# Optimization experiments

Measured on AMD Instinct MI355X. Metric: run time of the kernel, lower is better.

The kernel has to match this reference:

```python
import jax, jax.numpy as jnp
import numpy as np

H, W = 1024, 2048
K_CENTERS = 32          # fixed-size stand-in for torch.nonzero(center_heatmap > 0)
ROAD_ID = 0             # cityscapes trainId for 'road'
THING_START = 11        # cityscapes thing classes are trainIds >= 11
LABEL_DIVISOR = 1000
FILTER_IDS = (10, 19)   # 'sky', 'ego vehicle' depth filter classes
EPS = 1e-8


def _group_instances(heat, off, sem):
    # heat: (H,W) f32, off: (2,H,W) f32 [dy,dx], sem: (1,H,W) int
    vals, idx = jax.lax.top_k(heat.reshape(-1), K_CENTERS)
    cy = (idx // W).astype(jnp.float32)
    cx = (idx % W).astype(jnp.float32)
    valid = vals > 0.0
    ys = jnp.arange(H, dtype=jnp.float32)[:, None] + off[0]   # (H,W)
    xs = jnp.arange(W, dtype=jnp.float32)[None, :] + off[1]   # (H,W)
    d2 = (ys[None] - cy[:, None, None]) ** 2 + (xs[None] - cx[:, None, None]) ** 2  # (K,H,W)
    d2 = jnp.where(valid[:, None, None], d2, jnp.inf)
    inst = (jnp.argmin(d2, axis=0) + 1).astype(sem.dtype)     # (H,W), 1-based instance ids
    thing = sem >= THING_START
    any_valid = jnp.any(valid)
    return jnp.where(thing & any_valid, sem * LABEL_DIVISOR + inst[None], sem)


def _surface_normal(p):
    # p: (1,3,H,W) camera-space points; central-difference cross-product stencil
    px = jnp.pad(p, ((0, 0), (0, 0), (0, 0), (1, 1)), mode='edge')
    py = jnp.pad(p, ((0, 0), (0, 0), (1, 1), (0, 0)), mode='edge')
    vx = px[:, :, :, 2:] - px[:, :, :, :-2]
    vy = py[:, :, 2:, :] - py[:, :, :-2, :]
    n = jnp.cross(vx, vy, axis=1)
    return n / (jnp.linalg.norm(n, axis=1, keepdims=True) + EPS)


def setup_inputs() -> dict:
    key = jax.random.key(0)
    k1, k2, k3, k4 = jax.random.split(key, 4)
    sem_seg = jax.random.randint(k1, (1, 1, H, W), 0, 19, dtype=jnp.int64)
    center_heatmap = jax.random.normal(k2, (1, 1, H, W), dtype=jnp.float32) - 3.0
    offsets = jax.random.normal(k3, (1, 2, H, W), dtype=jnp.float32) * 5.0
    depth_logits = jax.random.uniform(k4, (1, 1, H, W), dtype=jnp.float32, minval=0.5, maxval=80.0)
    K_mat = np.array([[2262.52, 0.0, 1096.98], [0.0, 2265.30, 513.14], [0.0, 0.0, 1.0]], dtype=np.float32)
    inverse_camera_matrix = jnp.asarray(np.linalg.inv(K_mat), dtype=jnp.float32)
    real_camera_height = jnp.ones((1,), dtype=jnp.float32) * 1.7
    return {"sem_seg": sem_seg, "center_heatmap": center_heatmap, "offsets": offsets,
            "depth_logits": depth_logits, "inverse_camera_matrix": inverse_camera_matrix,
            "real_camera_height": real_camera_height}


def reference(sem_seg, center_heatmap, offsets, depth_logits, inverse_camera_matrix, real_camera_height):
    sem = sem_seg[0]                       # (1,H,W) int
    sem = _group_instances(center_heatmap[0, 0], offsets[0], sem)
    # pixel grid -> normalized camera rays
    xm = jnp.broadcast_to(jnp.arange(W, dtype=jnp.float32)[None, :], (H, W))
    ym = jnp.broadcast_to(jnp.arange(H, dtype=jnp.float32)[:, None], (H, W))
    grid = jnp.stack([xm, ym, jnp.ones((H, W), jnp.float32)], axis=0)           # (3,H,W)
    xnorm = jnp.einsum('ij,jhw->ihw', inverse_camera_matrix, grid)[None]        # (1,3,H,W)
    cam_points = xnorm * depth_logits                                           # (1,3,H,W)
    ground = sem == ROAD_ID                                                     # (1,H,W)
    normal = _surface_normal(cam_points)
    cam_heights = jnp.abs(jnp.sum(cam_points * normal, axis=1))                 # (1,H,W)
    # masked lower-median (torch.median semantics): sort with inf padding
    vals = jnp.where(ground, cam_heights, jnp.inf).reshape(-1)
    cnt = jnp.sum(ground.astype(jnp.int32))
    med_idx = jnp.maximum((cnt - 1) // 2, 0)
    cam_height = jnp.sort(vals)[med_idx]
    scale = real_camera_height.reshape(()) / cam_height
    depth = depth_logits * scale
    cam_points = cam_points * scale
    filt = (sem == FILTER_IDS[0])
    for cid in FILTER_IDS[1:]:
        filt = filt | (sem == cid)
    depth = jnp.where(filt[:, None], 0.0, depth)                                # (1,1,H,W)
    cam_out = jnp.concatenate([cam_points[0], sem.astype(jnp.float32)], axis=0).transpose(1, 2, 0)  # (H,W,4)
    return sem.astype(jnp.int32), depth[0], cam_out
```

## Files before the change

kernel.cpp:

```cpp
#include <hip/hip_runtime.h>
#include <math.h>

#define HH 1024
#define WW 2048
#define HW (HH*WW)
#define KC 32
#define NW 8192
#define CREGW 8
#define KCAP 12288
#define SENT 0xFFFFFFFFu
#define BIAS 16777216.0f

typedef unsigned long long u64;

struct Scratch {
  unsigned hist0[2048];
  unsigned hist1[2048];
  unsigned hist2[2048];
  unsigned done0;
  int nvalid;
  float scale;
  float ck[KC], m2cy[KC], m2cx[KC];
  unsigned ccnt[NW];
  unsigned cblk[NW];
};

__device__ __forceinline__ unsigned agent_load(const unsigned* p){
  return __hip_atomic_load(p, __ATOMIC_RELAXED, __HIP_MEMORY_SCOPE_AGENT);
}

template<int CTRL>
__device__ __forceinline__ u64 dpp_mov64(u64 x){
  unsigned lo = (unsigned)x, hi = (unsigned)(x>>32);
  unsigned nlo = (unsigned)__builtin_amdgcn_update_dpp((int)lo, (int)lo, CTRL, 0xF, 0xF, false);
  unsigned nhi = (unsigned)__builtin_amdgcn_update_dpp((int)hi, (int)hi, CTRL, 0xF, 0xF, false);
  return ((u64)nhi<<32) | (u64)nlo;
}
__device__ __forceinline__ u64 wave_max64(u64 x){
  u64 y;
  y = dpp_mov64<0x111>(x); if (y > x) x = y;
  y = dpp_mov64<0x112>(x); if (y > x) x = y;
  y = dpp_mov64<0x114>(x); if (y > x) x = y;
  y = dpp_mov64<0x118>(x); if (y > x) x = y;
  y = dpp_mov64<0x142>(x); if (y > x) x = y;
  y = dpp_mov64<0x143>(x); if (y > x) x = y;
  unsigned mlo = (unsigned)__builtin_amdgcn_readlane((int)(unsigned)x, 63);
  unsigned mhi = (unsigned)__builtin_amdgcn_readlane((int)(unsigned)(x>>32), 63);
  return ((u64)mhi<<32) | (u64)mlo;
}

#define CSWAP(a,b) { if ((b) > (a)) { u64 _t=(a); (a)=(b); (b)=_t; } }

__device__ __forceinline__ void grid_bar(unsigned* ctr, unsigned target){
  __syncthreads();
  if (threadIdx.x == 0){
    atomicAdd(ctr, 1u);
    while (__hip_atomic_load(ctr, __ATOMIC_RELAXED, __HIP_MEMORY_SCOPE_AGENT) < target)
      __builtin_amdgcn_s_sleep(2);
  }
  __syncthreads();
}

template<int PASS>
__device__ __forceinline__ void pick512(const unsigned* gh, unsigned* wsumL, unsigned* res){
  int t = threadIdx.x;
  unsigned v0 = agent_load(&gh[t*4+0]);
  unsigned v1 = agent_load(&gh[t*4+1]);
  unsigned v2 = agent_load(&gh[t*4+2]);
  unsigned v3 = agent_load(&gh[t*4+3]);
  int kin_prev = (PASS==0) ? 0 : (int)res[1];
  unsigned s = v0+v1+v2+v3;
  unsigned incl = s;
  #pragma unroll
  for (int d=1; d<64; d<<=1){ unsigned o = __shfl_up(incl, d); if ((t&63) >= d) incl += o; }
  unsigned excl = incl - s;
  if ((t&63)==63) wsumL[t>>6] = incl;
  __syncthreads();
  unsigned woff=0, total=0;
  #pragma unroll
  for (int w=0;w<8;w++){ unsigned xw=wsumL[w]; if (w < (t>>6)) woff += xw; total += xw; }
  unsigned pre = woff + excl;
  int k = (PASS==0) ? ((total>0) ? (int)((total-1)>>1) : 0) : kin_prev;
  if (total>0 && (unsigned)k >= pre && (unsigned)k < pre + s){
    unsigned kr = (unsigned)k - pre;
    int b_ = t*4;
    if (kr >= v0){ kr -= v0; b_++;
      if (kr >= v1){ kr -= v1; b_++;
        if (kr >= v2){ kr -= v2; b_++; } } }
    res[0] = (unsigned)b_; res[1] = kr;
  }
  if (t==0) res[2] = total;
  __syncthreads();
}

__global__ __launch_bounds__(256) void kA(const float* __restrict__ heat,
    const int* __restrict__ sem, const float* __restrict__ depth,
    const float* __restrict__ invK, u64* __restrict__ cand,
    unsigned* __restrict__ cheight, Scratch* __restrict__ sc){
  int t = threadIdx.x;
  if (blockIdx.x == 0){
    unsigned* hz = sc->hist0;
    for (int j=t; j<6144; j+=256) hz[j] = 0u;
    if (t==0) sc->done0 = 0u;
  }
  int i4 = blockIdx.x*256 + t;
  int p = i4<<2;
  int y = p>>11, x = p&2047;
  int row = y<<11;
  int lane = t & 63;
  unsigned wid = (unsigned)(blockIdx.x*4 + (t>>6));

  float4 hq = ((const float4*)heat)[i4];
  int4   s4 = ((const int4*)sem)[i4];
  float4 dc = ((const float4*)depth)[i4];
  float  dl = depth[row + (x>0 ? x-1 : 0)];
  float  dr = depth[row + (x+4<WW ? x+4 : WW-1)];
  int rowu = (y>0)?    row-WW : row;
  int rowd = (y<HH-1)? row+WW : row;
  float4 du = ((const float4*)(depth + rowu))[x>>2];
  float4 dd = ((const float4*)(depth + rowd))[x>>2];
  float ik0=invK[0],ik1=invK[1],ik2=invK[2];
  float ik3=invK[3],ik4=invK[4],ik5=invK[5];
  float ik6=invK[6],ik7=invK[7],ik8=invK[8];

  float hv[4] = {hq.x,hq.y,hq.z,hq.w};
  int   sv[4] = {s4.x,s4.y,s4.z,s4.w};
  float dcv[4]= {dc.x,dc.y,dc.z,dc.w};
  float duv[4]= {du.x,du.y,du.z,du.w};
  float ddv[4]= {dd.x,dd.y,dd.z,dd.w};

  unsigned npos = 0, ng = 0;
  #pragma unroll
  for (int j=0;j<4;j++){ npos += (hv[j] > 0.0f) ? 1u : 0u; ng += (sv[j]==0) ? 1u : 0u; }
  unsigned incc = npos, incg = ng;
  #pragma unroll
  for (int d=1; d<64; d<<=1){
    unsigned oc = __shfl_up(incc, d), og = __shfl_up(incg, d);
    if (lane >= d){ incc += oc; incg += og; }
  }

  float fy = (float)y;
  float a0=ik1*fy+ik2, a1=ik4*fy+ik5, a2=ik7*fy+ik8;
  float fyu=(y>0)?    fy-1.0f : fy;
  float fyd=(y<HH-1)? fy+1.0f : fy;
  float uu0=ik1*fyu+ik2, uu1=ik4*fyu+ik5, uu2=ik7*fyu+ik8;
  float ww0=ik1*fyd+ik2, ww1=ik4*fyd+ik5, ww2=ik7*fyd+ik8;
  float dxmv[4] = {dl, dcv[0], dcv[1], dcv[2]};
  float dxpv[4] = {dcv[1], dcv[2], dcv[3], dr};
  float h[4];
  #pragma unroll
  for (int j=0;j<4;j++){
    float fx  = (float)(x+j);
    float fxm = (x+j>0)?    fx-1.0f : fx;
    float fxp = (x+j<WW-1)? fx+1.0f : fx;
    float pc0=(ik0*fx +a0)*dcv[j],  pc1=(ik3*fx +a1)*dcv[j],  pc2=(ik6*fx +a2)*dcv[j];
    float pm0=(ik0*fxm+a0)*dxmv[j], pm1=(ik3*fxm+a1)*dxmv[j], pm2=(ik6*fxm+a2)*dxmv[j];
    float pp0=(ik0*fxp+a0)*dxpv[j], pp1=(ik3*fxp+a1)*dxpv[j], pp2=(ik6*fxp+a2)*dxpv[j];
    float pu0=(ik0*fx+uu0)*duv[j],  pu1=(ik3*fx+uu1)*duv[j],  pu2=(ik6*fx+uu2)*duv[j];
    float pd0=(ik0*fx+ww0)*ddv[j],  pd1=(ik3*fx+ww1)*ddv[j],  pd2=(ik6*fx+ww2)*ddv[j];
    float vx0=pp0-pm0, vx1=pp1-pm1, vx2=pp2-pm2;
    float vy0=pd0-pu0, vy1=pd1-pu1, vy2=pd2-pu2;
    float n0=vx1*vy2-vx2*vy1, n1=vx2*vy0-vx0*vy2, n2=vx0*vy1-vx1*vy0;
    float nn = sqrtf(n0*n0+n1*n1+n2*n2) + 1e-8f;
    h[j] = fabsf(pc0*n0+pc1*n1+pc2*n2) / nn;
  }

  if (npos){
    unsigned cslot = incc - npos;
    u64* cb = cand + ((size_t)wid * CREGW);
    #pragma unroll
    for (int j=0;j<4;j++){
      if (hv[j] > 0.0f){
        if (cslot < CREGW)
          cb[cslot] = ((u64)__float_as_uint(hv[j])<<32) | (u64)(unsigned)(~(unsigned)(p+j));
        cslot++;
      }
    }
  }
  if (ng){
    unsigned gslot = (wid<<8) + (incg - ng);
    #pragma unroll
    for (int j=0;j<4;j++){
      if (sv[j]==0){ cheight[gslot++] = __float_as_uint(h[j]); }
    }
  }
  if (lane == 63){
    sc->ccnt[wid] = (incc > CREGW) ? CREGW : incc;
    sc->cblk[wid] = incg;
  }
}

__global__ __launch_bounds__(64) void k_top(const u64* __restrict__ cand,
    const Scratch* __restrict__ sc, u64* __restrict__ tour){
  __shared__ unsigned cnt32[32];
  int lane = threadIdx.x;
  int b = blockIdx.x, r0 = b*32;
  if (lane < 32) cnt32[lane] = sc->ccnt[r0+lane];
  __syncthreads();
  int s0 = lane*4;
  u64 t0 = ((s0&7)     < cnt32[s0>>3])     ? cand[(size_t)r0*CREGW + s0]   : 0ULL;
  u64 t1 = (((s0+1)&7) < cnt32[(s0+1)>>3]) ? cand[(size_t)r0*CREGW + s0+1] : 0ULL;
  u64 t2 = (((s0+2)&7) < cnt32[(s0+2)>>3]) ? cand[(size_t)r0*CREGW + s0+2] : 0ULL;
  u64 t3 = (((s0+3)&7) < cnt32[(s0+3)>>3]) ? cand[(size_t)r0*CREGW + s0+3] : 0ULL;
  if (__ballot((t0|t1|t2|t3) != 0ULL) == 0ULL){
    if (lane < 32) tour[b*32 + lane] = 0ULL;
    return;
  }
  CSWAP(t0,t1) CSWAP(t2,t3) CSWAP(t0,t2) CSWAP(t1,t3) CSWAP(t1,t2)
  for (int r=0;r<32;r++){
    u64 m = wave_max64(t0);
    if (lane==0) tour[b*32+r] = m;
    if (m && t0==m){ t0=t1; t1=t2; t2=t3; t3=0ULL; }
  }
}

__global__ __launch_bounds__(512) void k_med(const unsigned* __restrict__ ch,
    const u64* __restrict__ tour, Scratch* __restrict__ sc,
    const float* __restrict__ rch){
  __shared__ unsigned keys[KCAP];
  __shared__ unsigned hsh[2048];
  __shared__ unsigned cnts[128], rstart[128], parr[128];
  __shared__ unsigned wsumL[8];
  __shared__ unsigned res[3];
  __shared__ unsigned misc[2];
  __shared__ u64 mls[4*KC];
  int t = threadIdx.x;
  int b = blockIdx.x;
  int lane = t & 63;
  int w = t >> 6;

  if (b == 64){
    u64 h0=0,h1=0,h2=0,h3=0;
    const u64* lp = tour + (size_t)(w*64+lane)*KC;
    if (w < 4){
      h0=lp[0]; h1=lp[1]; h2=lp[2]; h3=lp[3];
      int pp = 0;
      for (int r=0;r<KC;r++){
        u64 m = wave_max64(h0);
        if (lane==0) mls[w*KC+r] = m;
        if (m && h0==m){ pp++; h0=h1; h1=h2; h2=h3; h3 = (pp+3<KC)? lp[pp+3] : 0ULL; }
      }
    }
    __syncthreads();
    if (w == 0){
      u64 key = (lane<4) ? mls[lane*KC] : 0ULL;
      int p2=0, kk=0;
      for (int r=0;r<KC;r++){
        u64 m = wave_max64(key);
        if (m){
          if (lane==0){
            unsigned idx = ~(unsigned)(m & 0xFFFFFFFFULL);
            float cy = (float)(idx >> 11), cx = (float)(idx & 2047u);
            sc->ck[r]   = cy*cy + cx*cx + BIAS;
            sc->m2cy[r] = -2.0f*cy;
            sc->m2cx[r] = -2.0f*cx;
          }
          if (key==m){ p2++; key = (p2<KC)? mls[lane*KC+p2] : 0ULL; }
          kk = r+1;
        }
      }
      if (lane==0) sc->nvalid = kk;
    }
    return;
  }

  int r0 = b * 128;
  if (t==0){ res[0]=0u; res[1]=0u; res[2]=0u; misc[1]=0u; }
  if (t < 128) cnts[t] = sc->cblk[r0 + t];
  __syncthreads();
  if (t < 128){
    unsigned c = cnts[t];
    unsigned inc = c;
    #pragma unroll
    for (int d=1; d<64; d<<=1){ unsigned o = __shfl_up(inc, d); if (lane >= d) inc += o; }
    parr[t] = inc;
  }
  __syncthreads();
  if (t < 128){
    unsigned inc = parr[t] + ((t>=64)? parr[63] : 0u);
    rstart[t] = (inc <= KCAP) ? (inc - cnts[t]) : SENT;
    if (inc <= KCAP) atomicMax(&misc[1], inc);
    if (t == 127) misc[0] = inc;
  }
  for (int j=t;j<2048;j+=512) hsh[j]=0u;
  __syncthreads();
  unsigned total = misc[0];
  bool anyov = (total > KCAP);
  unsigned nl = anyov ? misc[1] : total;

  for (int k=0;k<16;k++){
    int r = w + (k<<3);
    unsigned c = cnts[r], rs = rstart[r];
    if (rs != SENT){
      const unsigned* base = ch + ((size_t)(r0+r)<<8);
      for (unsigned i=lane; i<c; i+=64) keys[rs+i] = base[i];
    }
  }
  __syncthreads();

  for (unsigned i=t; i<nl; i+=512) atomicAdd(&hsh[keys[i]>>21], 1u);
  if (anyov){
    for (int r=0;r<128;r++){
      if (rstart[r]==SENT){
        unsigned c = cnts[r];
        const unsigned* base = ch + ((size_t)(r0+r)<<8);
        for (unsigned i=t;i<c;i+=512) atomicAdd(&hsh[base[i]>>21], 1u);
      }
    }
  }
  __syncthreads();
  for (int j=t;j<2048;j+=512){ unsigned v=hsh[j]; if (v) atomicAdd(&sc->hist0[j], v); }
  grid_bar(&sc->done0, 64);
  pick512<0>(sc->hist0, wsumL, res);
  unsigned tot0 = res[2];
  unsigned pref0 = res[0];
  for (int j=t;j<2048;j+=512) hsh[j]=0u;
  __syncthreads();

  for (unsigned i=t; i<nl; i+=512){
    unsigned key = keys[i];
    if ((key>>21) == pref0) atomicAdd(&hsh[(key>>10)&2047u], 1u);
  }
  if (anyov){
    for (int r=0;r<128;r++){
      if (rstart[r]==SENT){
        unsigned c = cnts[r];
        const unsigned* base = ch + ((size_t)(r0+r)<<8);
        for (unsigned i=t;i<c;i+=512){ unsigned key=base[i]; if ((key>>21)==pref0) atomicAdd(&hsh[(key>>10)&2047u], 1u); }
      }
    }
  }
  __syncthreads();
  for (int j=t;j<2048;j+=512){ unsigned v=hsh[j]; if (v) atomicAdd(&sc->hist1[j], v); }
  grid_bar(&sc->done0, 128);
  pick512<1>(sc->hist1, wsumL, res);
  unsigned pref01 = (pref0 << 11) | res[0];
  for (int j=t;j<2048;j+=512) hsh[j]=0u;
  __syncthreads();

  for (unsigned i=t; i<nl; i+=512){
    unsigned key = keys[i];
    if ((key>>10) == pref01) atomicAdd(&hsh[key & 1023u], 1u);
  }
  if (anyov){
    for (int r=0;r<128;r++){
      if (rstart[r]==SENT){
        unsigned c = cnts[r];
        const unsigned* base = ch + ((size_t)(r0+r)<<8);
        for (unsigned i=t;i<c;i+=512){ unsigned key=base[i]; if ((key>>10)==pref01) atomicAdd(&hsh[key & 1023u], 1u); }
      }
    }
  }
  __syncthreads();
  for (int j=t;j<2048;j+=512){ unsigned v=hsh[j]; if (v) atomicAdd(&sc->hist2[j], v); }
  grid_bar(&sc->done0, 192);
  pick512<2>(sc->hist2, wsumL, res);
  if (b == 0 && t == 0){
    unsigned key = (pref01 << 10) | res[0];
    sc->scale = (tot0 > 0) ? (rch[0] / __uint_as_float(key)) : 0.0f;
  }
}

__global__ __launch_bounds__(256) void k_final(const int* __restrict__ sem,
    const float* __restrict__ off, const float* __restrict__ depth,
    const float* __restrict__ invK, const Scratch* __restrict__ sc,
    float* __restrict__ out){
  __shared__ float sck[KC], smy[KC], smx[KC];
  __shared__ int snv; __shared__ float ssc;
  int t = threadIdx.x;
  if (t < KC){ sck[t]=sc->ck[t]; smy[t]=sc->m2cy[t]; smx[t]=sc->m2cx[t]; }
  if (t == 0){ snv = sc->nvalid; ssc = sc->scale; }
  __syncthreads();

  int i4 = blockIdx.x*256 + t;
  int p = i4<<2;
  int y = p>>11, x = p&2047;
  int4   s4 = ((const int4*)sem)[i4];
  float4 oy = ((const float4*)off)[i4];
  float4 ox = ((const float4*)(off+HW))[i4];
  float4 dc = ((const float4*)depth)[i4];

  float ik0=invK[0],ik1=invK[1],ik2=invK[2];
  float ik3=invK[3],ik4=invK[4],ik5=invK[5];
  float ik6=invK[6],ik7=invK[7],ik8=invK[8];
  float fy = (float)y;
  float a0=ik1*fy+ik2, a1=ik4*fy+ik5, a2=ik7*fy+ik8;
  int nv = snv; float s = ssc;

  int   sv[4]  = {s4.x,s4.y,s4.z,s4.w};
  float oyv[4] = {oy.x,oy.y,oy.z,oy.w};
  float oxv[4] = {ox.x,ox.y,ox.z,ox.w};
  float dv[4]  = {dc.x,dc.y,dc.z,dc.w};

  float ys[4], xs[4]; unsigned ub[4];
  #pragma unroll
  for (int j=0;j<4;j++){
    ys[j] = fy + oyv[j]; xs[j] = (float)(x+j) + oxv[j]; ub[j] = SENT;
  }
  for (int k=0;k<nv;k++){
    float ckk=sck[k], my=smy[k], mx=smx[k];
    #pragma unroll
    for (int j=0;j<4;j++){
      float tt = fmaf(ys[j], my, ckk);
      tt = fmaf(xs[j], mx, tt);
      unsigned uu = (__float_as_uint(tt) & ~31u) | (unsigned)k;
      ub[j] = uu < ub[j] ? uu : ub[j];
    }
  }
  float lab[4], depo[4];
  float4* cam = (float4*)(out + (size_t)2*HW);
  #pragma unroll
  for (int j=0;j<4;j++){
    int sj = sv[j];
    lab[j] = (sj >= 11 && nv > 0) ? (float)(sj*1000 + (int)(ub[j]&31u) + 1) : (float)sj;
    float fx = (float)(x+j);
    float ds = dv[j]*s;
    float p0=(ik0*fx+a0)*ds, p1=(ik3*fx+a1)*ds, p2=(ik6*fx+a2)*ds;
    bool filt = (lab[j]==10.0f) || (lab[j]==19.0f);
    depo[j] = filt ? 0.0f : ds;
    cam[p+j] = make_float4(p0, p1, p2, lab[j]);
  }
  ((float4*)out)[i4]      = make_float4(lab[0], lab[1], lab[2], lab[3]);
  ((float4*)(out+HW))[i4] = make_float4(depo[0], depo[1], depo[2], depo[3]);
}

extern "C" void kernel_launch(void* const* d_in, const int* in_sizes, int n_in,
                              void* d_out, int out_size, void* d_ws, size_t ws_size,
                              hipStream_t stream){
  const int*   sem   = (const int*)d_in[0];
  const float* heat  = (const float*)d_in[1];
  const float* off   = (const float*)d_in[2];
  const float* depth = (const float*)d_in[3];
  const float* invK  = (const float*)d_in[4];
  const float* rch   = (const float*)d_in[5];
  float* out = (float*)d_out;

  unsigned* cheight = (unsigned*)d_ws;
  u64* cand = (u64*)((char*)d_ws + (size_t)NW*256*4);
  u64* tour = (u64*)((char*)d_ws + (size_t)NW*256*4 + (size_t)NW*CREGW*8);
  Scratch* sc = (Scratch*)((char*)d_ws + (size_t)NW*256*4 + (size_t)NW*CREGW*8 + (size_t)256*KC*8);

  const int grid4 = HW/4/256;

  kA<<<grid4, 256, 0, stream>>>(heat, sem, depth, invK, cand, cheight, sc);
  k_top<<<256, 64, 0, stream>>>(cand, sc, tour);
  k_med<<<65, 512, 0, stream>>>(cheight, tour, sc, rch);
  k_final<<<grid4, 256, 0, stream>>>(sem, off, depth, invK, sc, out);
}
```

Before: 61.53 us.

## Merge top-k tournament and median kernels into one launch, doubling median blocks

```diff
diff --git a/kernel.cpp b/kernel.cpp
--- a/kernel.cpp
+++ b/kernel.cpp
@@ -8,6 +8,7 @@
 #define NW 8192
 #define CREGW 8
 #define KCAP 12288
+#define NMED 128
 #define SENT 0xFFFFFFFFu
 #define BIAS 16777216.0f
 
@@ -17,7 +18,7 @@
   unsigned hist0[2048];
   unsigned hist1[2048];
   unsigned hist2[2048];
-  unsigned done0;
+  unsigned done0, doneA;
   int nvalid;
   float scale;
   float ck[KC], m2cy[KC], m2cx[KC];
@@ -27,6 +28,12 @@
 
 __device__ __forceinline__ unsigned agent_load(const unsigned* p){
   return __hip_atomic_load(p, __ATOMIC_RELAXED, __HIP_MEMORY_SCOPE_AGENT);
+}
+__device__ __forceinline__ u64 agent_load64(const u64* p){
+  return __hip_atomic_load(p, __ATOMIC_RELAXED, __HIP_MEMORY_SCOPE_AGENT);
+}
+__device__ __forceinline__ void agent_store64(u64* p, u64 v){
+  __hip_atomic_store(p, v, __ATOMIC_RELAXED, __HIP_MEMORY_SCOPE_AGENT);
 }
 
 template<int CTRL>
@@ -101,7 +108,7 @@
   if (blockIdx.x == 0){
     unsigned* hz = sc->hist0;
     for (int j=t; j<6144; j+=256) hz[j] = 0u;
-    if (t==0) sc->done0 = 0u;
+    if (t==0){ sc->done0 = 0u; sc->doneA = 0u; }
   }
   int i4 = blockIdx.x*256 + t;
   int p = i4<<2;
@@ -190,97 +197,96 @@
   }
 }
 
-__global__ __launch_bounds__(64) void k_top(const u64* __restrict__ cand,
-    const Scratch* __restrict__ sc, u64* __restrict__ tour){
-  __shared__ unsigned cnt32[32];
-  int lane = threadIdx.x;
-  int b = blockIdx.x, r0 = b*32;
-  if (lane < 32) cnt32[lane] = sc->ccnt[r0+lane];
-  __syncthreads();
-  int s0 = lane*4;
-  u64 t0 = ((s0&7)     < cnt32[s0>>3])     ? cand[(size_t)r0*CREGW + s0]   : 0ULL;
-  u64 t1 = (((s0+1)&7) < cnt32[(s0+1)>>3]) ? cand[(size_t)r0*CREGW + s0+1] : 0ULL;
-  u64 t2 = (((s0+2)&7) < cnt32[(s0+2)>>3]) ? cand[(size_t)r0*CREGW + s0+2] : 0ULL;
-  u64 t3 = (((s0+3)&7) < cnt32[(s0+3)>>3]) ? cand[(size_t)r0*CREGW + s0+3] : 0ULL;
-  if (__ballot((t0|t1|t2|t3) != 0ULL) == 0ULL){
-    if (lane < 32) tour[b*32 + lane] = 0ULL;
-    return;
-  }
-  CSWAP(t0,t1) CSWAP(t2,t3) CSWAP(t0,t2) CSWAP(t1,t3) CSWAP(t1,t2)
-  for (int r=0;r<32;r++){
-    u64 m = wave_max64(t0);
-    if (lane==0) tour[b*32+r] = m;
-    if (m && t0==m){ t0=t1; t1=t2; t2=t3; t3=0ULL; }
-  }
-}
-
-__global__ __launch_bounds__(512) void k_med(const unsigned* __restrict__ ch,
-    const u64* __restrict__ tour, Scratch* __restrict__ sc,
-    const float* __restrict__ rch){
+__global__ __launch_bounds__(512) void k_ms(const unsigned* __restrict__ ch,
+    const u64* __restrict__ cand, u64* __restrict__ tour,
+    Scratch* __restrict__ sc, const float* __restrict__ rch){
   __shared__ unsigned keys[KCAP];
   __shared__ unsigned hsh[2048];
-  __shared__ unsigned cnts[128], rstart[128], parr[128];
+  __shared__ unsigned cnts[64], rstart[64];
   __shared__ unsigned wsumL[8];
   __shared__ unsigned res[3];
   __shared__ unsigned misc[2];
   __shared__ u64 mls[4*KC];
+  __shared__ int lastA;
   int t = threadIdx.x;
   int b = blockIdx.x;
   int lane = t & 63;
   int w = t >> 6;
 
-  if (b == 64){
-    u64 h0=0,h1=0,h2=0,h3=0;
-    const u64* lp = tour + (size_t)(w*64+lane)*KC;
-    if (w < 4){
-      h0=lp[0]; h1=lp[1]; h2=lp[2]; h3=lp[3];
-      int pp = 0;
-      for (int r=0;r<KC;r++){
-        u64 m = wave_max64(h0);
-        if (lane==0) mls[w*KC+r] = m;
-        if (m && h0==m){ pp++; h0=h1; h1=h2; h2=h3; h3 = (pp+3<KC)? lp[pp+3] : 0ULL; }
+  if (b < 256){
+    if (t < 64){
+      int r0 = b*32;
+      if (lane < 32) cnts[lane] = sc->ccnt[r0+lane];
+      int s0 = lane*4;
+      unsigned c0c = __shfl(cnts[0], 0); (void)c0c;
+      u64 t0=0,t1=0,t2=0,t3=0;
+      t0 = ((s0&7)     < cnts[s0>>3])     ? cand[(size_t)r0*CREGW + s0]   : 0ULL;
+      t1 = (((s0+1)&7) < cnts[(s0+1)>>3]) ? cand[(size_t)r0*CREGW + s0+1] : 0ULL;
+      t2 = (((s0+2)&7) < cnts[(s0+2)>>3]) ? cand[(size_t)r0*CREGW + s0+2] : 0ULL;
+      t3 = (((s0+3)&7) < cnts[(s0+3)>>3]) ? cand[(size_t)r0*CREGW + s0+3] : 0ULL;
+      if (__ballot((t0|t1|t2|t3) != 0ULL) == 0ULL){
+        if (lane < 32) agent_store64(&tour[b*32 + lane], 0ULL);
+      } else {
+        CSWAP(t0,t1) CSWAP(t2,t3) CSWAP(t0,t2) CSWAP(t1,t3) CSWAP(t1,t2)
+        for (int r=0;r<32;r++){
+          u64 m = wave_max64(t0);
+          if (lane==0) agent_store64(&tour[b*32+r], m);
+          if (m && t0==m){ t0=t1; t1=t2; t2=t3; t3=0ULL; }
+        }
       }
     }
     __syncthreads();
-    if (w == 0){
-      u64 key = (lane<4) ? mls[lane*KC] : 0ULL;
-      int p2=0, kk=0;
-      for (int r=0;r<KC;r++){
-        u64 m = wave_max64(key);
-        if (m){
-          if (lane==0){
-            unsigned idx = ~(unsigned)(m & 0xFFFFFFFFULL);
-            float cy = (float)(idx >> 11), cx = (float)(idx & 2047u);
-            sc->ck[r]   = cy*cy + cx*cx + BIAS;
-            sc->m2cy[r] = -2.0f*cy;
-            sc->m2cx[r] = -2.0f*cx;
+    if (t==0) lastA = (atomicAdd(&sc->doneA, 1u) == 255u) ? 1 : 0;
+    __syncthreads();
+    if (lastA){
+      const u64* lp = tour + (size_t)(w*64+lane)*KC;
+      if (w < 4){
+        u64 h0=agent_load64(&lp[0]), h1=agent_load64(&lp[1]);
+        u64 h2=agent_load64(&lp[2]), h3=agent_load64(&lp[3]);
+        int pp = 0;
+        for (int r=0;r<KC;r++){
+          u64 m = wave_max64(h0);
+          if (lane==0) mls[w*KC+r] = m;
+          if (m && h0==m){ pp++; h0=h1; h1=h2; h2=h3; h3 = (pp+3<KC)? agent_load64(&lp[pp+3]) : 0ULL; }
+        }
+      }
+      __syncthreads();
+      if (w == 0){
+        u64 key = (lane<4) ? mls[lane*KC] : 0ULL;
+        int p2=0, kk=0;
+        for (int r=0;r<KC;r++){
+          u64 m = wave_max64(key);
+          if (m){
+            if (lane==0){
+              unsigned idx = ~(unsigned)(m & 0xFFFFFFFFULL);
+              float cy = (float)(idx >> 11), cx = (float)(idx & 2047u);
+              sc->ck[r]   = cy*cy + cx*cx + BIAS;
+              sc->m2cy[r] = -2.0f*cy;
+              sc->m2cx[r] = -2.0f*cx;
+            }
+            if (key==m){ p2++; key = (p2<KC)? mls[lane*KC+p2] : 0ULL; }
+            kk = r+1;
           }
-          if (key==m){ p2++; key = (p2<KC)? mls[lane*KC+p2] : 0ULL; }
-          kk = r+1;
         }
-      }
-      if (lane==0) sc->nvalid = kk;
+        if (lane==0) sc->nvalid = kk;
+      }
     }
     return;
   }
 
-  int r0 = b * 128;
+  int mb = b - 256;
+  int r0 = mb * 64;
   if (t==0){ res[0]=0u; res[1]=0u; res[2]=0u; misc[1]=0u; }
-  if (t < 128) cnts[t] = sc->cblk[r0 + t];
-  __syncthreads();
-  if (t < 128){
-    unsigned c = cnts[t];
+  __syncthreads();
+  if (t < 64){
+    unsigned c = sc->cblk[r0 + t];
+    cnts[t] = c;
     unsigned inc = c;
     #pragma unroll
     for (int d=1; d<64; d<<=1){ unsigned o = __shfl_up(inc, d); if (lane >= d) inc += o; }
-    parr[t] = inc;
-  }
-  __syncthreads();
-  if (t < 128){
-    unsigned inc = parr[t] + ((t>=64)? parr[63] : 0u);
-    rstart[t] = (inc <= KCAP) ? (inc - cnts[t]) : SENT;
+    rstart[t] = (inc <= KCAP) ? (inc - c) : SENT;
     if (inc <= KCAP) atomicMax(&misc[1], inc);
-    if (t == 127) misc[0] = inc;
+    if (t == 63) misc[0] = inc;
   }
   for (int j=t;j<2048;j+=512) hsh[j]=0u;
   __syncthreads();
@@ -288,7 +294,8 @@
   bool anyov = (total > KCAP);
   unsigned nl = anyov ? misc[1] : total;
 
-  for (int k=0;k<16;k++){
+  #pragma unroll
+  for (int k=0;k<8;k++){
     int r = w + (k<<3);
     unsigned c = cnts[r], rs = rstart[r];
     if (rs != SENT){
@@ -300,7 +307,7 @@
 
   for (unsigned i=t; i<nl; i+=512) atomicAdd(&hsh[keys[i]>>21], 1u);
   if (anyov){
-    for (int r=0;r<128;r++){
+    for (int r=0;r<64;r++){
       if (rstart[r]==SENT){
         unsigned c = cnts[r];
         const unsigned* base = ch + ((size_t)(r0+r)<<8);
@@ -310,7 +317,7 @@
   }
   __syncthreads();
   for (int j=t;j<2048;j+=512){ unsigned v=hsh[j]; if (v) atomicAdd(&sc->hist0[j], v); }
-  grid_bar(&sc->done0, 64);
+  grid_bar(&sc->done0, NMED);
   pick512<0>(sc->hist0, wsumL, res);
   unsigned tot0 = res[2];
   unsigned pref0 = res[0];
@@ -322,7 +329,7 @@
     if ((key>>21) == pref0) atomicAdd(&hsh[(key>>10)&2047u], 1u);
   }
   if (anyov){
-    for (int r=0;r<128;r++){
+    for (int r=0;r<64;r++){
       if (rstart[r]==SENT){
         unsigned c = cnts[r];
         const unsigned* base = ch + ((size_t)(r0+r)<<8);
@@ -332,7 +339,7 @@
   }
   __syncthreads();
   for (int j=t;j<2048;j+=512){ unsigned v=hsh[j]; if (v) atomicAdd(&sc->hist1[j], v); }
-  grid_bar(&sc->done0, 128);
+  grid_bar(&sc->done0, 2*NMED);
   pick512<1>(sc->hist1, wsumL, res);
   unsigned pref01 = (pref0 << 11) | res[0];
   for (int j=t;j<2048;j+=512) hsh[j]=0u;
@@ -343,7 +350,7 @@
     if ((key>>10) == pref01) atomicAdd(&hsh[key & 1023u], 1u);
   }
   if (anyov){
-    for (int r=0;r<128;r++){
+    for (int r=0;r<64;r++){
       if (rstart[r]==SENT){
         unsigned c = cnts[r];
         const unsigned* base = ch + ((size_t)(r0+r)<<8);
@@ -353,9 +360,9 @@
   }
   __syncthreads();
   for (int j=t;j<2048;j+=512){ unsigned v=hsh[j]; if (v) atomicAdd(&sc->hist2[j], v); }
-  grid_bar(&sc->done0, 192);
+  grid_bar(&sc->done0, 3*NMED);
   pick512<2>(sc->hist2, wsumL, res);
-  if (b == 0 && t == 0){
+  if (mb == 0 && t == 0){
     unsigned key = (pref01 << 10) | res[0];
     sc->scale = (tot0 > 0) ? (rch[0] / __uint_as_float(key)) : 0.0f;
   }
@@ -443,7 +450,6 @@
   const int grid4 = HW/4/256;
 
   kA<<<grid4, 256, 0, stream>>>(heat, sem, depth, invK, cand, cheight, sc);
-  k_top<<<256, 64, 0, stream>>>(cand, sc, tour);
-  k_med<<<65, 512, 0, stream>>>(cheight, tour, sc, rch);
+  k_ms<<<256+NMED, 512, 0, stream>>>(cheight, cand, tour, sc, rch);
   k_final<<<grid4, 256, 0, stream>>>(sem, off, depth, invK, sc, out);
 }
```

Result: slower. 67.87 us (+10.3%).
